# Kernel optimization log

Measured on AMD Instinct MI355X. Metric: run time of the kernel, lower is better.

The kernel has to match this reference:

```python
import jax, jax.numpy as jnp
import numpy as np

N_ENT = 50000     # n_entities
C = 128           # channel
N_EDGES = 1600000 # n_edges (avg degree 32)
N_REL = 11        # n_relations; edge_type in [1, N_REL-1]
N_HOPS = 3
EPS = 1e-12       # F.normalize default eps


def setup_inputs() -> dict:
    key = jax.random.key(0)
    k1, k2, k3, k4 = jax.random.split(key, 4)
    entity_emb = jax.random.normal(k1, (N_ENT, C), dtype=jnp.float32)
    edge_index = jax.random.randint(k2, (2, N_EDGES), 0, N_ENT, dtype=jnp.int64)
    edge_type = jax.random.randint(k3, (N_EDGES,), 1, N_REL, dtype=jnp.int64)
    # xavier_uniform bound for (N_REL-1, C)
    bound = float(np.sqrt(6.0 / ((N_REL - 1) + C)))
    weight = jax.random.uniform(k4, (N_REL - 1, C), jnp.float32, -bound, bound)
    return {"entity_emb": entity_emb, "edge_index": edge_index,
            "edge_type": edge_type, "weight": weight}


def reference(entity_emb, edge_index, edge_type, weight):
    head, tail = edge_index[0], edge_index[1]
    # relation embedding per edge: weight[edge_type - 1] -> [E, C]
    rel_emb = weight[edge_type - 1]
    ones = jnp.ones((edge_index.shape[1],), entity_emb.dtype)
    # per-head in-degree counts (constant across hops)
    cnt = jax.ops.segment_sum(ones, head, num_segments=N_ENT)
    denom = jnp.maximum(cnt, 1.0)[:, None]  # scatter_mean: zero rows stay zero

    def hop(emb):
        msg = emb[tail] * rel_emb                                   # gather + mul [E, C]
        agg = jax.ops.segment_sum(msg, head, num_segments=N_ENT) / denom  # scatter_mean
        # F.normalize (L2 per row)
        norm = jnp.linalg.norm(agg, axis=1, keepdims=True)
        return agg / jnp.maximum(norm, EPS)

    res = entity_emb
    emb = entity_emb
    for _ in range(N_HOPS):
        emb = hop(emb)
        res = res + emb
    return res
```

## Files before the change

kernel.cpp:

```cpp
#include <hip/hip_runtime.h>

#define N_ENT   50000
#define CH      128
#define N_EDGES 1600000
#define N_RELM1 10
#define NB      391
#define BCAP    4608
#define BCAP_P  8192
#define PART_BLOCKS 800
#define CHUNK   (N_EDGES / PART_BLOCKS)
#define NRG     (N_ENT / 4)
#define NKEY    512
#define EPS_N   1e-12f

#define RFL(x) __builtin_amdgcn_readfirstlane(x)

__device__ __forceinline__ unsigned int f2bf_bits(float f) {
    unsigned int x = __float_as_uint(f);
    return (x + 0x7FFFu + ((x >> 16) & 1u)) >> 16;
}

__global__ __launch_bounds__(256) void gc_part_kernel(const int* __restrict__ head,
                                                      const int* __restrict__ tail,
                                                      const int* __restrict__ etyp,
                                                      int* __restrict__ barr,
                                                      int* __restrict__ pack,
                                                      const float* __restrict__ ent,
                                                      unsigned int* __restrict__ emb) {
    __shared__ int hist[512];
    __shared__ int boff_s[512];
    __shared__ int fctr[512];
    __shared__ int psum[256];
    __shared__ int stageE[CHUNK];
    __shared__ unsigned short stageB[CHUNK];
    __shared__ int stage2[CHUNK];
    int tid = threadIdx.x, blk = blockIdx.x;
    for (int i = tid; i < 512; i += 256) { hist[i] = 0; fctr[i] = 0; }
    __syncthreads();
    int lo = blk * CHUNK;
    for (int i = tid; i < CHUNK; i += 256) {
        int e = lo + i;
        int h = head[e];
        int b = h >> 7;
        stageE[i] = (tail[e] & 0xFFFF) | ((etyp[e] - 1) << 16) | ((h & 127) << 20);
        stageB[i] = (unsigned short)b;
        atomicAdd(&hist[b], 1);
    }
    __syncthreads();
    int a0 = hist[2 * tid], a1 = hist[2 * tid + 1];
    int s2 = a0 + a1;
    psum[tid] = s2;
    __syncthreads();
    for (int d = 1; d < 256; d <<= 1) {
        int t = (tid >= d) ? psum[tid - d] : 0;
        __syncthreads();
        psum[tid] += t;
        __syncthreads();
    }
    int excl = psum[tid] - s2;
    boff_s[2 * tid] = excl;
    boff_s[2 * tid + 1] = excl + a0;
    __syncthreads();
    for (int i = tid; i < CHUNK; i += 256) {
        int b = stageB[i];
        int pos = boff_s[b] + atomicAdd(&fctr[b], 1);
        stage2[pos] = stageE[i];
    }
    __syncthreads();
    for (int i = tid; i < CHUNK; i += 256) barr[lo + i] = stage2[i];
    for (int i = tid; i < NB; i += 256)
        pack[blk * NB + i] = (boff_s[i] << 8) | fctr[i];
    for (int i = blk * 256 + tid; i < N_ENT * (CH / 2); i += PART_BLOCKS * 256) {
        float2 v = *(const float2*)(ent + 2 * (size_t)i);
        emb[i] = f2bf_bits(v.x) | (f2bf_bits(v.y) << 16);
    }
}

__global__ __launch_bounds__(1024) void gc_place_kernel(const int* __restrict__ barr,
                                                        const int* __restrict__ pack,
                                                        int* __restrict__ deg_arr,
                                                        int* __restrict__ rg_off,
                                                        int* __restrict__ cpk,
                                                        int* __restrict__ csr) {
    __shared__ int ent_s[BCAP];
    __shared__ int psum[1024];
    __shared__ int kcnt[NKEY];
    __shared__ int kctr[NKEY];
    __shared__ int kbase[NKEY];
    int b = blockIdx.x, tid = threadIdx.x;
    if (tid < NKEY) { kcnt[tid] = 0; kctr[tid] = 0; }
    int c = 0, o = 0;
    if (tid < PART_BLOCKS) {
        int pk = pack[tid * NB + b];
        c = pk & 255;
        o = pk >> 8;
    }
    psum[tid] = c;
    __syncthreads();
    for (int d = 1; d < 1024; d <<= 1) {
        int t = (tid >= d) ? psum[tid - d] : 0;
        __syncthreads();
        psum[tid] += t;
        __syncthreads();
    }
    int my_off = psum[tid] - c;
    int n = psum[1023];
    const int* src = barr + tid * CHUNK + o;
    for (int k = 0; k < c; ++k) ent_s[my_off + k] = src[k];
    __syncthreads();
    for (int i = tid; i < n; i += 1024) {
        int e = ent_s[i];
        int hl = (e >> 20) & 127;
        int key = ((hl >> 2) << 4) | (((e >> 14) & 3) << 2) | (hl & 3);
        atomicAdd(&kcnt[key], 1);
    }
    __syncthreads();
    if (tid < 128) {
        int rgl = tid >> 2, r = tid & 3;
        int base = (rgl << 4) | r;
        int c0 = kcnt[base], c1 = kcnt[base + 4], c2 = kcnt[base + 8], c3 = kcnt[base + 12];
        int h = (b << 7) + tid;
        if (h < N_ENT) {
            deg_arr[h] = c0 + c1 + c2 + c3;
            cpk[(((b << 5) + rgl) << 2) + r] =
                ((c0 + 7) >> 3) | (((c1 + 7) >> 3) << 8) |
                (((c2 + 7) >> 3) << 16) | (((c3 + 7) >> 3) << 24);
        }
    }
    int a0 = 0, a1 = 0, s2 = 0;
    if (tid < 256) {
        a0 = (kcnt[2 * tid] + 7) & ~7;
        a1 = (kcnt[2 * tid + 1] + 7) & ~7;
        s2 = a0 + a1;
        psum[tid] = s2;
    }
    __syncthreads();
    for (int d = 1; d < 256; d <<= 1) {
        int t = (tid < 256 && tid >= d) ? psum[tid - d] : 0;
        __syncthreads();
        if (tid < 256) psum[tid] += t;
        __syncthreads();
    }
    if (tid < 256) {
        int excl = psum[tid] - s2;
        kbase[2 * tid] = excl;
        kbase[2 * tid + 1] = excl + a0;
    }
    __syncthreads();
    int lo = b * BCAP_P;
    if (tid < 32) {
        int grg = (b << 5) + tid;
        if (grg < NRG) rg_off[grg] = lo + kbase[tid << 4];
    }
    for (int i = tid; i < n; i += 1024) {
        int e = ent_s[i];
        int hl = (e >> 20) & 127;
        int key = ((hl >> 2) << 4) | (((e >> 14) & 3) << 2) | (hl & 3);
        int pos = lo + kbase[key] + atomicAdd(&kctr[key], 1);
        csr[pos] = e & 0xFFFFF;
    }
    __syncthreads();
    if (tid < NKEY) {
        int cc = kcnt[tid];
        int pc = (cc + 7) & ~7;
        int p0 = lo + kbase[tid];
        for (int k = cc; k < pc; ++k) csr[p0 + k] = 15 << 16;
    }
}

__global__ __launch_bounds__(256, 8) void gc_hop_kernel(
        const unsigned int* __restrict__ src,
        const int* __restrict__ deg_arr,
        const int* __restrict__ rg_off,
        const int* __restrict__ cpk,
        const int* __restrict__ csr,
        const float* __restrict__ wt,
        unsigned int* __restrict__ dst,
        float* __restrict__ res,
        const float* __restrict__ ent,
        const unsigned int* __restrict__ yprev,
        int mode) {
    __shared__ float wt_s[16 * CH];
    for (int i = threadIdx.x; i < 16 * CH; i += 256)
        wt_s[i] = (i < N_RELM1 * CH) ? wt[i] : 0.f;
    __syncthreads();

    int wave = threadIdx.x >> 6, lane = threadIdx.x & 63;
    int rg = RFL(blockIdx.x * 4 + wave);
    if (rg >= NRG) return;

    int4 dd = ((const int4*)deg_arr)[rg];
    int4 cc = ((const int4*)cpk)[rg];
    int segv = rg_off[rg];

    int D0 = RFL(dd.x), D1 = RFL(dd.y), D2 = RFL(dd.z), D3 = RFL(dd.w);
    int C0 = RFL(cc.x), C1 = RFL(cc.y), C2 = RFL(cc.z), C3 = RFL(cc.w);
    int seg = RFL(segv);

    const int4* mp = (const int4*)(csr + seg);

    float ax0 = 0.f, ay0 = 0.f, ax1 = 0.f, ay1 = 0.f;
    float ax2 = 0.f, ay2 = 0.f, ax3 = 0.f, ay3 = 0.f;

    const unsigned* srcl = src + lane;
    const float2*   wl   = (const float2*)wt_s + lane;

#define CHUNK8(axr, ayr) { \
    int4 m0_ = mp[0], m1_ = mp[1]; mp += 2; \
    int p0_ = RFL(m0_.x), p1_ = RFL(m0_.y), p2_ = RFL(m0_.z), p3_ = RFL(m0_.w); \
    int p4_ = RFL(m1_.x), p5_ = RFL(m1_.y), p6_ = RFL(m1_.z), p7_ = RFL(m1_.w); \
    unsigned v0_ = srcl[(unsigned)(p0_ & 0xFFFF) * 64u]; \
    unsigned v1_ = srcl[(unsigned)(p1_ & 0xFFFF) * 64u]; \
    unsigned v2_ = srcl[(unsigned)(p2_ & 0xFFFF) * 64u]; \
    unsigned v3_ = srcl[(unsigned)(p3_ & 0xFFFF) * 64u]; \
    unsigned v4_ = srcl[(unsigned)(p4_ & 0xFFFF) * 64u]; \
    unsigned v5_ = srcl[(unsigned)(p5_ & 0xFFFF) * 64u]; \
    unsigned v6_ = srcl[(unsigned)(p6_ & 0xFFFF) * 64u]; \
    unsigned v7_ = srcl[(unsigned)(p7_ & 0xFFFF) * 64u]; \
    float2 w0_ = wl[((p0_ >> 16) & 15) * 64]; \
    float2 w1_ = wl[((p1_ >> 16) & 15) * 64]; \
    float2 w2_ = wl[((p2_ >> 16) & 15) * 64]; \
    float2 w3_ = wl[((p3_ >> 16) & 15) * 64]; \
    float2 w4_ = wl[((p4_ >> 16) & 15) * 64]; \
    float2 w5_ = wl[((p5_ >> 16) & 15) * 64]; \
    float2 w6_ = wl[((p6_ >> 16) & 15) * 64]; \
    float2 w7_ = wl[((p7_ >> 16) & 15) * 64]; \
    axr = fmaf(__uint_as_float(v0_ << 16), w0_.x, axr); \
    ayr = fmaf(__uint_as_float(v0_ & 0xFFFF0000u), w0_.y, ayr); \
    axr = fmaf(__uint_as_float(v1_ << 16), w1_.x, axr); \
    ayr = fmaf(__uint_as_float(v1_ & 0xFFFF0000u), w1_.y, ayr); \
    axr = fmaf(__uint_as_float(v2_ << 16), w2_.x, axr); \
    ayr = fmaf(__uint_as_float(v2_ & 0xFFFF0000u), w2_.y, ayr); \
    axr = fmaf(__uint_as_float(v3_ << 16), w3_.x, axr); \
    ayr = fmaf(__uint_as_float(v3_ & 0xFFFF0000u), w3_.y, ayr); \
    axr = fmaf(__uint_as_float(v4_ << 16), w4_.x, axr); \
    ayr = fmaf(__uint_as_float(v4_ & 0xFFFF0000u), w4_.y, ayr); \
    axr = fmaf(__uint_as_float(v5_ << 16), w5_.x, axr); \
    ayr = fmaf(__uint_as_float(v5_ & 0xFFFF0000u), w5_.y, ayr); \
    axr = fmaf(__uint_as_float(v6_ << 16), w6_.x, axr); \
    ayr = fmaf(__uint_as_float(v6_ & 0xFFFF0000u), w6_.y, ayr); \
    axr = fmaf(__uint_as_float(v7_ << 16), w7_.x, axr); \
    ayr = fmaf(__uint_as_float(v7_ & 0xFFFF0000u), w7_.y, ayr); \
}

#define RUN(axr, ayr, Cr) { \
    int n_ = (Cr >> sh) & 255; \
    for (int c_ = 0; c_ < n_; ++c_) CHUNK8(axr, ayr) \
}

    for (int g2 = 0; g2 < 4; ++g2) {
        int sh = g2 << 3;
        RUN(ax0, ay0, C0)
        RUN(ax1, ay1, C1)
        RUN(ax2, ay2, C2)
        RUN(ax3, ay3, C3)
    }
#undef RUN
#undef CHUNK8

#define ROWOUT(r, axr, ayr, Dr) { \
        int row = (rg << 2) + r; \
        float invd = 1.0f / fmaxf((float)Dr, 1.0f); \
        float x0 = axr * invd, x1 = ayr * invd; \
        float s = x0 * x0 + x1 * x1; \
        _Pragma("unroll") \
        for (int o = 32; o; o >>= 1) s += __shfl_xor(s, o, 64); \
        float inv = 1.0f / fmaxf(sqrtf(s), EPS_N); \
        float y0 = x0 * inv, y1v = x1 * inv; \
        if (mode == 0) { \
            dst[(row << 6) + lane] = f2bf_bits(y0) | (f2bf_bits(y1v) << 16); \
        } else { \
            unsigned p1 = yprev[(row << 6) + lane]; \
            unsigned p2 = src[(row << 6) + lane]; \
            int base = (row << 7) + 2 * lane; \
            float2 e = *(const float2*)(ent + base); \
            float2 o2; \
            o2.x = e.x + __uint_as_float(p1 << 16) \
                       + __uint_as_float(p2 << 16) + y0; \
            o2.y = e.y + __uint_as_float(p1 & 0xFFFF0000u) \
                       + __uint_as_float(p2 & 0xFFFF0000u) + y1v; \
            *(float2*)(res + base) = o2; \
        } }

    ROWOUT(0, ax0, ay0, D0);
    ROWOUT(1, ax1, ay1, D1);
    ROWOUT(2, ax2, ay2, D2);
    ROWOUT(3, ax3, ay3, D3);
#undef ROWOUT
}

extern "C" void kernel_launch(void* const* d_in, const int* in_sizes, int n_in,
                              void* d_out, int out_size, void* d_ws, size_t ws_size,
                              hipStream_t stream) {
    const float* ent  = (const float*)d_in[0];
    const int*   eidx = (const int*)d_in[1];
    const int*   etyp = (const int*)d_in[2];
    const float* wt   = (const float*)d_in[3];
    float*       res  = (float*)d_out;

    const int* head = eidx;
    const int* tail = eidx + N_EDGES;

    unsigned int* embA = (unsigned int*)d_ws;
    unsigned int* embB = embA + (size_t)N_ENT * 64;
    int* barr = (int*)embB;
    int* pack = (int*)embB + N_EDGES;
    int* deg_arr = (int*)(embB + (size_t)N_ENT * 64);
    int* rg_off  = deg_arr + N_ENT;
    int* cpk     = rg_off + 12544;
    int* csr     = cpk + (size_t)NRG * 4;

    gc_part_kernel<<<PART_BLOCKS, 256, 0, stream>>>(head, tail, etyp, barr, pack,
                                                    ent, embA);
    gc_place_kernel<<<NB, 1024, 0, stream>>>(barr, pack, deg_arr, rg_off, cpk, csr);

    const int hop_grid = NRG / 4;
    gc_hop_kernel<<<hop_grid, 256, 0, stream>>>(embA, deg_arr, rg_off, cpk, csr,
                                                wt, embB, res, ent, embB, 0);
    gc_hop_kernel<<<hop_grid, 256, 0, stream>>>(embB, deg_arr, rg_off, cpk, csr,
                                                wt, embA, res, ent, embB, 0);
    gc_hop_kernel<<<hop_grid, 256, 0, stream>>>(embA, deg_arr, rg_off, cpk, csr,
                                                wt, embB, res, ent, embB, 1);
}
```

Baseline: 265.3 us.

## Replace two-pass block partition with global histogram, scan, and atomic scatter CSR build

The CSR construction moves from a per-block bucket partition followed by a per-bucket placement kernel to a global atomic histogram over the final bins. A small per-bucket scan computes the padded bin bases and bin cursors, and a separate scatter kernel places each edge with a global atomic on its bin cursor. This removes the intermediate barr/pack buffers and the large shared-memory staging. The cost is many contended global atomics, an extra memset and launch, and reading the edge arrays twice.

```diff
diff --git a/kernel.cpp b/kernel.cpp
--- a/kernel.cpp
+++ b/kernel.cpp
@@ -5,12 +5,10 @@
 #define N_EDGES 1600000
 #define N_RELM1 10
 #define NB      391
-#define BCAP    4608
 #define BCAP_P  8192
-#define PART_BLOCKS 800
-#define CHUNK   (N_EDGES / PART_BLOCKS)
 #define NRG     (N_ENT / 4)
 #define NKEY    512
+#define NBIN    (NB * NKEY)
 #define EPS_N   1e-12f
 
 #define RFL(x) __builtin_amdgcn_readfirstlane(x)
@@ -20,105 +18,71 @@
     return (x + 0x7FFFu + ((x >> 16) & 1u)) >> 16;
 }
 
-__global__ __launch_bounds__(256) void gc_part_kernel(const int* __restrict__ head,
-                                                      const int* __restrict__ tail,
-                                                      const int* __restrict__ etyp,
-                                                      int* __restrict__ barr,
-                                                      int* __restrict__ pack,
-                                                      const float* __restrict__ ent,
-                                                      unsigned int* __restrict__ emb) {
-    __shared__ int hist[512];
-    __shared__ int boff_s[512];
-    __shared__ int fctr[512];
-    __shared__ int psum[256];
-    __shared__ int stageE[CHUNK];
-    __shared__ unsigned short stageB[CHUNK];
-    __shared__ int stage2[CHUNK];
-    int tid = threadIdx.x, blk = blockIdx.x;
-    for (int i = tid; i < 512; i += 256) { hist[i] = 0; fctr[i] = 0; }
-    __syncthreads();
-    int lo = blk * CHUNK;
-    for (int i = tid; i < CHUNK; i += 256) {
-        int e = lo + i;
-        int h = head[e];
-        int b = h >> 7;
-        stageE[i] = (tail[e] & 0xFFFF) | ((etyp[e] - 1) << 16) | ((h & 127) << 20);
-        stageB[i] = (unsigned short)b;
-        atomicAdd(&hist[b], 1);
-    }
-    __syncthreads();
-    int a0 = hist[2 * tid], a1 = hist[2 * tid + 1];
-    int s2 = a0 + a1;
-    psum[tid] = s2;
-    __syncthreads();
-    for (int d = 1; d < 256; d <<= 1) {
-        int t = (tid >= d) ? psum[tid - d] : 0;
-        __syncthreads();
-        psum[tid] += t;
-        __syncthreads();
-    }
-    int excl = psum[tid] - s2;
-    boff_s[2 * tid] = excl;
-    boff_s[2 * tid + 1] = excl + a0;
-    __syncthreads();
-    for (int i = tid; i < CHUNK; i += 256) {
-        int b = stageB[i];
-        int pos = boff_s[b] + atomicAdd(&fctr[b], 1);
-        stage2[pos] = stageE[i];
-    }
-    __syncthreads();
-    for (int i = tid; i < CHUNK; i += 256) barr[lo + i] = stage2[i];
-    for (int i = tid; i < NB; i += 256)
-        pack[blk * NB + i] = (boff_s[i] << 8) | fctr[i];
-    for (int i = blk * 256 + tid; i < N_ENT * (CH / 2); i += PART_BLOCKS * 256) {
+__global__ __launch_bounds__(256) void gc_count_kernel(const int* __restrict__ head,
+                                                       const int* __restrict__ tail,
+                                                       const int* __restrict__ etyp,
+                                                       int* __restrict__ ghist,
+                                                       const float* __restrict__ ent,
+                                                       unsigned int* __restrict__ emb) {
+    int stride = gridDim.x * 256;
+    for (int e = blockIdx.x * 256 + threadIdx.x; e < N_EDGES; e += stride) {
+        int h = head[e], t = tail[e];
+        int bin = ((h >> 2) << 4) | (((t >> 14) & 3) << 2) | (h & 3);
+        atomicAdd(&ghist[bin], 1);
+    }
+    for (int i = blockIdx.x * 256 + threadIdx.x; i < N_ENT * (CH / 2); i += stride) {
         float2 v = *(const float2*)(ent + 2 * (size_t)i);
         emb[i] = f2bf_bits(v.x) | (f2bf_bits(v.y) << 16);
     }
 }
 
-__global__ __launch_bounds__(1024) void gc_place_kernel(const int* __restrict__ barr,
-                                                        const int* __restrict__ pack,
-                                                        int* __restrict__ deg_arr,
-                                                        int* __restrict__ rg_off,
-                                                        int* __restrict__ cpk,
-                                                        int* __restrict__ csr) {
-    __shared__ int ent_s[BCAP];
-    __shared__ int psum[1024];
+__global__ __launch_bounds__(256) void gc_scan_kernel(const int* __restrict__ ghist,
+                                                      int* __restrict__ kcur,
+                                                      int* __restrict__ deg_arr,
+                                                      int* __restrict__ rg_off,
+                                                      int* __restrict__ cpk,
+                                                      int* __restrict__ csr) {
     __shared__ int kcnt[NKEY];
-    __shared__ int kctr[NKEY];
     __shared__ int kbase[NKEY];
+    __shared__ int wsum[4];
     int b = blockIdx.x, tid = threadIdx.x;
-    if (tid < NKEY) { kcnt[tid] = 0; kctr[tid] = 0; }
-    int c = 0, o = 0;
-    if (tid < PART_BLOCKS) {
-        int pk = pack[tid * NB + b];
-        c = pk & 255;
-        o = pk >> 8;
-    }
-    psum[tid] = c;
-    __syncthreads();
-    for (int d = 1; d < 1024; d <<= 1) {
-        int t = (tid >= d) ? psum[tid - d] : 0;
-        __syncthreads();
-        psum[tid] += t;
-        __syncthreads();
-    }
-    int my_off = psum[tid] - c;
-    int n = psum[1023];
-    const int* src = barr + tid * CHUNK + o;
-    for (int k = 0; k < c; ++k) ent_s[my_off + k] = src[k];
-    __syncthreads();
-    for (int i = tid; i < n; i += 1024) {
-        int e = ent_s[i];
-        int hl = (e >> 20) & 127;
-        int key = ((hl >> 2) << 4) | (((e >> 14) & 3) << 2) | (hl & 3);
-        atomicAdd(&kcnt[key], 1);
-    }
-    __syncthreads();
+    int gb = b * NKEY;
+    kcnt[tid] = ghist[gb + tid];
+    kcnt[tid + 256] = ghist[gb + tid + 256];
+    __syncthreads();
+    int a0 = (kcnt[2 * tid] + 7) & ~7;
+    int a1 = (kcnt[2 * tid + 1] + 7) & ~7;
+    int v = a0 + a1;
+    int lane = tid & 63, wid = tid >> 6;
+    int inc = v;
+    #pragma unroll
+    for (int d = 1; d < 64; d <<= 1) {
+        int t = __shfl_up(inc, d, 64);
+        if (lane >= d) inc += t;
+    }
+    if (lane == 63) wsum[wid] = inc;
+    __syncthreads();
+    int woff = 0;
+    for (int i = 0; i < wid; ++i) woff += wsum[i];
+    int excl = woff + inc - v;
+    kbase[2 * tid] = excl;
+    kbase[2 * tid + 1] = excl + a0;
+    __syncthreads();
+    int lo = b * BCAP_P;
+    #pragma unroll
+    for (int k = 0; k < 2; ++k) {
+        int bin = 2 * tid + k;
+        int cc = kcnt[bin];
+        int base = lo + kbase[bin];
+        kcur[gb + bin] = base;
+        int pc = (cc + 7) & ~7;
+        for (int j = cc; j < pc; ++j) csr[base + j] = 15 << 16;
+    }
     if (tid < 128) {
         int rgl = tid >> 2, r = tid & 3;
         int base = (rgl << 4) | r;
-        int c0 = kcnt[base], c1 = kcnt[base + 4], c2 = kcnt[base + 8], c3 = kcnt[base + 12];
+        int c0 = kcnt[base], c1 = kcnt[base + 4];
+        int c2 = kcnt[base + 8], c3 = kcnt[base + 12];
         int h = (b << 7) + tid;
         if (h < N_ENT) {
             deg_arr[h] = c0 + c1 + c2 + c3;
@@ -127,44 +91,23 @@
                 (((c2 + 7) >> 3) << 16) | (((c3 + 7) >> 3) << 24);
         }
     }
-    int a0 = 0, a1 = 0, s2 = 0;
-    if (tid < 256) {
-        a0 = (kcnt[2 * tid] + 7) & ~7;
-        a1 = (kcnt[2 * tid + 1] + 7) & ~7;
-        s2 = a0 + a1;
-        psum[tid] = s2;
-    }
-    __syncthreads();
-    for (int d = 1; d < 256; d <<= 1) {
-        int t = (tid < 256 && tid >= d) ? psum[tid - d] : 0;
-        __syncthreads();
-        if (tid < 256) psum[tid] += t;
-        __syncthreads();
-    }
-    if (tid < 256) {
-        int excl = psum[tid] - s2;
-        kbase[2 * tid] = excl;
-        kbase[2 * tid + 1] = excl + a0;
-    }
-    __syncthreads();
-    int lo = b * BCAP_P;
     if (tid < 32) {
         int grg = (b << 5) + tid;
         if (grg < NRG) rg_off[grg] = lo + kbase[tid << 4];
     }
-    for (int i = tid; i < n; i += 1024) {
-        int e = ent_s[i];
-        int hl = (e >> 20) & 127;
-        int key = ((hl >> 2) << 4) | (((e >> 14) & 3) << 2) | (hl & 3);
-        int pos = lo + kbase[key] + atomicAdd(&kctr[key], 1);
-        csr[pos] = e & 0xFFFFF;
-    }
-    __syncthreads();
-    if (tid < NKEY) {
-        int cc = kcnt[tid];
-        int pc = (cc + 7) & ~7;
-        int p0 = lo + kbase[tid];
-        for (int k = cc; k < pc; ++k) csr[p0 + k] = 15 << 16;
+}
+
+__global__ __launch_bounds__(256) void gc_scatter_kernel(const int* __restrict__ head,
+                                                         const int* __restrict__ tail,
+                                                         const int* __restrict__ etyp,
+                                                         int* __restrict__ kcur,
+                                                         int* __restrict__ csr) {
+    int stride = gridDim.x * 256;
+    for (int e = blockIdx.x * 256 + threadIdx.x; e < N_EDGES; e += stride) {
+        int h = head[e], t = tail[e], ty = etyp[e];
+        int bin = ((h >> 2) << 4) | (((t >> 14) & 3) << 2) | (h & 3);
+        int pos = atomicAdd(&kcur[bin], 1);
+        csr[pos] = (t & 0xFFFF) | ((ty - 1) << 16);
     }
 }
 
@@ -303,16 +246,17 @@
 
     unsigned int* embA = (unsigned int*)d_ws;
     unsigned int* embB = embA + (size_t)N_ENT * 64;
-    int* barr = (int*)embB;
-    int* pack = (int*)embB + N_EDGES;
-    int* deg_arr = (int*)(embB + (size_t)N_ENT * 64);
+    int* csr     = (int*)(embB + (size_t)N_ENT * 64);
+    int* deg_arr = csr + (size_t)NB * BCAP_P;
     int* rg_off  = deg_arr + N_ENT;
     int* cpk     = rg_off + 12544;
-    int* csr     = cpk + (size_t)NRG * 4;
-
-    gc_part_kernel<<<PART_BLOCKS, 256, 0, stream>>>(head, tail, etyp, barr, pack,
-                                                    ent, embA);
-    gc_place_kernel<<<NB, 1024, 0, stream>>>(barr, pack, deg_arr, rg_off, cpk, csr);
+    int* ghist   = cpk + (size_t)NRG * 4;
+    int* kcur    = ghist + NBIN;
+
+    hipMemsetAsync(ghist, 0, NBIN * sizeof(int), stream);
+    gc_count_kernel<<<1024, 256, 0, stream>>>(head, tail, etyp, ghist, ent, embA);
+    gc_scan_kernel<<<NB, 256, 0, stream>>>(ghist, kcur, deg_arr, rg_off, cpk, csr);
+    gc_scatter_kernel<<<2048, 256, 0, stream>>>(head, tail, etyp, kcur, csr);
 
     const int hop_grid = NRG / 4;
     gc_hop_kernel<<<hop_grid, 256, 0, stream>>>(embA, deg_arr, rg_off, cpk, csr,
```

Measured after the change: 436.6 us. 64.6% more time.
